# Kernel tuning notes

Measured on AMD Instinct MI355X. Metric: run time of the kernel, lower is better.

The kernel has to match this reference:

```python
import jax, jax.numpy as jnp
import numpy as np

# ---- static config (mirrors HashEncoderHyFluid.__init__) ----
MIN_RES = np.array([16, 16, 16, 16], dtype=np.float64)
MAX_RES = np.array([256, 256, 256, 128], dtype=np.float64)
NUM_SCALES = 16
MAX_PARAMS = 2 ** 19
F = 2  # features_per_level
N_QUERIES = 1_000_000
PRIMES = np.array([1, 2654435761, 805459861, 3674653429], dtype=np.uint32)
# 16 corner offsets of the 4D hypercube, bit d of idx selects low/high along dim d
BITS = np.array([[(i >> d) & 1 for d in range(4)] for i in range(16)], dtype=np.int32)  # (16,4)


def build_config():
    b = np.exp((np.log(MAX_RES) - np.log(MIN_RES)) / (NUM_SCALES - 1))
    shapes, sizes, indicators, offsets = [], [], [], []
    total = 0
    for s in range(NUM_SCALES):
        res = np.ceil(MIN_RES * np.power(b, s)).astype(np.int64)
        raw = int(res[0] + 1) * int(res[1] + 1) * int(res[2] + 1) * int(res[3] + 1)
        p = raw if raw % 8 == 0 else ((raw + 7) // 8) * 8
        p = min(MAX_PARAMS, p)
        shapes.append(res)
        sizes.append(p)
        indicators.append(1 if raw <= p else 0)
        offsets.append(total)
        total += p * F
    return shapes, sizes, indicators, offsets, total


SHAPES, SIZES, INDICATORS, OFFSETS, TOTAL_HASH_SIZE = build_config()  # total = 15205344


def setup_inputs() -> dict:
    key = jax.random.key(0)
    k1, k2 = jax.random.split(key)
    xyzt = jax.random.uniform(k1, (N_QUERIES, 4), dtype=jnp.float32)  # coords in [0,1)
    hash_table = (jax.random.uniform(k2, (TOTAL_HASH_SIZE,), dtype=jnp.float32) * 2.0 - 1.0) * 0.001
    return {"xyzt": xyzt, "hash_table": hash_table}


def _encode_scale(xyzt, hash_table, res, size, indicator, offset):
    # xyzt: (N,4) in [0,1]; res: np int64 (4,)
    resf = jnp.asarray(res.astype(np.float32))
    pos = xyzt * resf                      # (N,4) grid-space position
    grid = jnp.floor(pos)
    frac = pos - grid                      # (N,4)
    grid = grid.astype(jnp.int32)
    corners = grid[:, None, :] + jnp.asarray(BITS)[None, :, :]          # (N,16,4)
    hi = jnp.asarray(BITS, jnp.float32)[None, :, :]                     # (1,16,4)
    w = jnp.prod(hi * frac[:, None, :] + (1.0 - hi) * (1.0 - frac[:, None, :]), axis=-1)  # (N,16)
    cu = corners.astype(jnp.uint32)
    if indicator == 1:
        # dense linear indexing: strides = cumprod(res+1), wrapping at uint32 like taichi
        strides = np.cumprod(np.concatenate([[1], (res + 1)[:3]])).astype(np.uint32)
        idx = jnp.sum(cu * jnp.asarray(strides), axis=-1)               # (N,16) uint32, wraps
    else:
        # xor hash with large primes
        h = cu[..., 0] * jnp.uint32(PRIMES[0])
        for d in range(1, 4):
            h = h ^ (cu[..., d] * jnp.uint32(PRIMES[d]))
        idx = h
    idx = (idx % jnp.uint32(size)).astype(jnp.int32)
    base = offset + idx * F                                             # (N,16)
    feats = hash_table[base[..., None] + jnp.arange(F)]                 # (N,16,F)
    return jnp.einsum("nc,ncf->nf", w, feats)                           # (N,F)


def reference(xyzt, hash_table):
    outs = []
    for s in range(NUM_SCALES):
        outs.append(_encode_scale(xyzt, hash_table, SHAPES[s], SIZES[s], INDICATORS[s], OFFSETS[s]))
    return jnp.concatenate(outs, axis=-1)  # (N, NUM_SCALES * F)
```

## Files before the change

kernel.cpp:

```cpp
#include <hip/hip_runtime.h>
#include <cstdint>
#include <cmath>


#define NSCALES 16
#define TPB 256
#define BINS 65536

struct Cfg {
  float    res[NSCALES][4];
  uint32_t key[NSCALES][4];
  uint32_t mask[NSCALES];
  int      offset[NSCALES];
  int      dense[NSCALES];
};

typedef float v4f __attribute__((ext_vector_type(4)));
typedef float v2f __attribute__((ext_vector_type(2)));

__device__ __forceinline__ uint32_t bucket_key(float x, float y, float z, float w)
{
  uint32_t bx = (uint32_t)(x * 16.f); bx = bx > 15u ? 15u : bx;
  uint32_t by = (uint32_t)(y * 16.f); by = by > 15u ? 15u : by;
  uint32_t bz = (uint32_t)(z * 16.f); bz = bz > 15u ? 15u : bz;
  uint32_t bt = (uint32_t)(w * 16.f); bt = bt > 15u ? 15u : bt;
  uint32_t k = 0;
#pragma unroll
  for (int b = 0; b < 4; ++b) {
    k |= ((bx >> b) & 1u) << (4 * b + 0);
    k |= ((by >> b) & 1u) << (4 * b + 1);
    k |= ((bz >> b) & 1u) << (4 * b + 2);
    k |= ((bt >> b) & 1u) << (4 * b + 3);
  }
  return k;
}

__global__ __launch_bounds__(TPB) void hist_kernel(
    const float* __restrict__ xyzt, uint32_t* __restrict__ hist, int N)
{
  const int i = blockIdx.x * TPB + threadIdx.x;
  if (i >= N) return;
  const v4f c = *(reinterpret_cast<const v4f*>(xyzt) + i);
  atomicAdd(&hist[bucket_key(c.x, c.y, c.z, c.w)], 1u);
}

__global__ __launch_bounds__(256) void scan_kernel(
    const uint32_t* __restrict__ hist, uint32_t* __restrict__ boff)
{
  __shared__ uint32_t part[256];
  const int t = threadIdx.x;
  const int base = t * (BINS / 256);
  uint32_t s = 0;
  for (int j = 0; j < BINS / 256; ++j) s += hist[base + j];
  part[t] = s;
  __syncthreads();
  for (int off = 1; off < 256; off <<= 1) {
    uint32_t v = (t >= off) ? part[t - off] : 0u;
    __syncthreads();
    part[t] += v;
    __syncthreads();
  }
  uint32_t run = part[t] - s;
  for (int j = 0; j < BINS / 256; ++j) {
    boff[base + j] = run;
    run += hist[base + j];
  }
}

__global__ __launch_bounds__(TPB) void scatter_kernel(
    const float* __restrict__ xyzt,
    const uint32_t* __restrict__ boff, uint32_t* __restrict__ cur,
    uint32_t* __restrict__ perm, float* __restrict__ c_sorted, int N)
{
  const int i = blockIdx.x * TPB + threadIdx.x;
  if (i >= N) return;
  const v4f c = *(reinterpret_cast<const v4f*>(xyzt) + i);
  const uint32_t k = bucket_key(c.x, c.y, c.z, c.w);
  const uint32_t pos = boff[k] + atomicAdd(&cur[k], 1u);
  perm[pos] = (uint32_t)i;
  *(reinterpret_cast<v4f*>(c_sorted) + pos) = c;
}

__global__ __launch_bounds__(TPB) void gather_kernel(
    const float*  __restrict__ coords,
    const float*  __restrict__ table,
    float2*       __restrict__ ws,
    int N, Cfg cfg)
{
  const int s = blockIdx.y;
  const int q = blockIdx.x * TPB + threadIdx.x;
  if (q >= N) return;
  const v4f c = *(reinterpret_cast<const v4f*>(coords) + q);

  const float rx = cfg.res[s][0], ry = cfg.res[s][1];
  const float rz = cfg.res[s][2], rw = cfg.res[s][3];
  const uint32_t K0 = cfg.key[s][0], K1 = cfg.key[s][1];
  const uint32_t K2 = cfg.key[s][2], K3 = cfg.key[s][3];

  const float px = c.x * rx, py = c.y * ry, pz = c.z * rz, pw = c.w * rw;
  const float gx = floorf(px), gy = floorf(py), gz = floorf(pz), gw = floorf(pw);
  const float fx = px - gx, fy = py - gy, fz = pz - gz, fw = pw - gw;
  const uint32_t ix = (uint32_t)(int)gx, iy = (uint32_t)(int)gy;
  const uint32_t iz = (uint32_t)(int)gz, iw = (uint32_t)(int)gw;

  const uint32_t x0 = ix * K0, x1 = x0 + K0;
  const uint32_t y0 = iy * K1, y1 = y0 + K1;
  const uint32_t z0 = iz * K2, z1 = z0 + K2;
  const uint32_t u0 = iw * K3, u1 = u0 + K3;

  const float wx0 = 1.f - fx, wy0 = 1.f - fy, wz0 = 1.f - fz, ww0 = 1.f - fw;
  const float wA[4] = { wx0 * wy0, fx * wy0, wx0 * fy, fx * fy };
  const float wB[4] = { wz0 * ww0, fz * ww0, wz0 * fw, fz * fw };

  const float*  tbf = table + cfg.offset[s];
  const float2* __restrict__ tb  = reinterpret_cast<const float2*>(tbf);
  const float4* __restrict__ tb4 = reinterpret_cast<const float4*>(tbf);

  float a0 = 0.f, a1 = 0.f;
  if (cfg.dense[s]) {
    const uint32_t hA[4] = { x0 + y0, x1 + y0, x0 + y1, x1 + y1 };
    const uint32_t hB[4] = { z0 + u0, z1 + u0, z0 + u1, z1 + u1 };
#pragma unroll
    for (int i = 0; i < 16; ++i) {
      const uint32_t idx = hA[i & 3] + hB[i >> 2];
      const float2 v = tb[idx];
      const float w = wA[i & 3] * wB[i >> 2];
      a0 = fmaf(w, v.x, a0);
      a1 = fmaf(w, v.y, a1);
    }
  } else {
    const uint32_t msk = cfg.mask[s];
    if ((ix & 1u) == 0u) {
      const uint32_t yv[2] = { y0, y1 };
      const uint32_t zw[4] = { z0 ^ u0, z1 ^ u0, z0 ^ u1, z1 ^ u1 };
#pragma unroll
      for (int j = 0; j < 8; ++j) {
        const int jy = j & 1, jz = j >> 1;
        const uint32_t p  = (x0 ^ yv[jy] ^ zw[jz]) & msk;
        const uint32_t e  = p & ~1u;
        const uint32_t sel = p & 1u;
        const float4 v = tb4[e >> 1];
        const float wlo = wA[2 * jy]     * wB[jz];
        const float whi = wA[2 * jy + 1] * wB[jz];
        const float l0 = sel ? v.z : v.x, l1 = sel ? v.w : v.y;
        const float h0 = sel ? v.x : v.z, h1 = sel ? v.y : v.w;
        a0 = fmaf(wlo, l0, fmaf(whi, h0, a0));
        a1 = fmaf(wlo, l1, fmaf(whi, h1, a1));
      }
    } else {
      const uint32_t hA[4] = { x0 ^ y0, x1 ^ y0, x0 ^ y1, x1 ^ y1 };
      const uint32_t hB[4] = { z0 ^ u0, z1 ^ u0, z0 ^ u1, z1 ^ u1 };
#pragma unroll
      for (int i = 0; i < 16; ++i) {
        const uint32_t idx = (hA[i & 3] ^ hB[i >> 2]) & msk;
        const float2 v = tb[idx];
        const float w = wA[i & 3] * wB[i >> 2];
        a0 = fmaf(w, v.x, a0);
        a1 = fmaf(w, v.y, a1);
      }
    }
  }
  v2f val = { a0, a1 };
  __builtin_nontemporal_store(val, (v2f*)&ws[(size_t)s * N + q]);
}

__global__ __launch_bounds__(TPB) void transpose_direct(
    const float2*   __restrict__ ws,
    const uint32_t* __restrict__ perm,
    float*          __restrict__ out,
    int N)
{
  const int g = blockIdx.x * TPB + threadIdx.x;
  if (g >= N * 8) return;
  const int q  = g >> 3;
  const int l8 = g & 7;
  const int s0 = l8 * 2;
  const float2 a = ws[(size_t)s0 * N + q];
  const float2 b = ws[(size_t)(s0 + 1) * N + q];
  const uint32_t pq = perm[q];
  v4f val = { a.x, a.y, b.x, b.y };
  __builtin_nontemporal_store(val, (v4f*)(out + (size_t)pq * 32 + l8 * 4));
}

__global__ __launch_bounds__(TPB) void transpose_kernel(
    const float2* __restrict__ ws,
    float*        __restrict__ out,
    int N)
{
  __shared__ float2 st[NSCALES][TPB + 1];
  const int t  = threadIdx.x;
  const int q  = blockIdx.x * TPB + t;
  const int ql = q < N ? q : N - 1;
#pragma unroll
  for (int s = 0; s < NSCALES; ++s)
    st[s][t] = ws[(size_t)s * N + ql];
  __syncthreads();
  const int base = blockIdx.x * (TPB * 2 * NSCALES);
#pragma unroll
  for (int it = 0; it < 8; ++it) {
    const int G  = it * 1024 + t * 4;
    const int qi = G >> 5;
    const int s0 = (G & 31) >> 1;
    if (blockIdx.x * TPB + qi < N) {
      const float2 a = st[s0][qi];
      const float2 b = st[s0 + 1][qi];
      v4f val = { a.x, a.y, b.x, b.y };
      __builtin_nontemporal_store(val, (v4f*)(out + base + G));
    }
  }
}

__global__ __launch_bounds__(TPB) void hashenc_fused(
    const float4* __restrict__ xyzt,
    const float*  __restrict__ table,
    float*        __restrict__ out,
    int N, Cfg cfg)
{
  __shared__ float2 st[NSCALES][TPB + 1];
  const int t  = threadIdx.x;
  const int q  = blockIdx.x * TPB + t;
  const int ql = q < N ? q : N - 1;
  const float4 c = xyzt[ql];
#pragma unroll 1
  for (int s = 0; s < NSCALES; ++s) {
    const float rx = cfg.res[s][0], ry = cfg.res[s][1];
    const float rz = cfg.res[s][2], rw = cfg.res[s][3];
    const uint32_t K0 = cfg.key[s][0], K1 = cfg.key[s][1];
    const uint32_t K2 = cfg.key[s][2], K3 = cfg.key[s][3];
    const float px = c.x * rx, py = c.y * ry, pz = c.z * rz, pw = c.w * rw;
    const float gx = floorf(px), gy = floorf(py), gz = floorf(pz), gw = floorf(pw);
    const float fx = px - gx, fy = py - gy, fz = pz - gz, fw = pw - gw;
    const uint32_t ix = (uint32_t)(int)gx, iy = (uint32_t)(int)gy;
    const uint32_t iz = (uint32_t)(int)gz, iw = (uint32_t)(int)gw;
    const uint32_t x0 = ix * K0, x1 = x0 + K0;
    const uint32_t y0 = iy * K1, y1 = y0 + K1;
    const uint32_t z0 = iz * K2, z1 = z0 + K2;
    const uint32_t u0 = iw * K3, u1 = u0 + K3;
    const float wx0 = 1.f - fx, wy0 = 1.f - fy, wz0 = 1.f - fz, ww0 = 1.f - fw;
    const float wA[4] = { wx0 * wy0, fx * wy0, wx0 * fy, fx * fy };
    const float wB[4] = { wz0 * ww0, fz * ww0, wz0 * fw, fz * fw };
    const float2* __restrict__ tb =
        reinterpret_cast<const float2*>(table + cfg.offset[s]);
    float a0 = 0.f, a1 = 0.f;
    if (cfg.dense[s]) {
      const uint32_t hA[4] = { x0 + y0, x1 + y0, x0 + y1, x1 + y1 };
      const uint32_t hB[4] = { z0 + u0, z1 + u0, z0 + u1, z1 + u1 };
#pragma unroll
      for (int i = 0; i < 16; ++i) {
        const uint32_t idx = hA[i & 3] + hB[i >> 2];
        const float2 v = tb[idx];
        const float w = wA[i & 3] * wB[i >> 2];
        a0 = fmaf(w, v.x, a0); a1 = fmaf(w, v.y, a1);
      }
    } else {
      const uint32_t msk = cfg.mask[s];
      const uint32_t hA[4] = { x0 ^ y0, x1 ^ y0, x0 ^ y1, x1 ^ y1 };
      const uint32_t hB[4] = { z0 ^ u0, z1 ^ u0, z0 ^ u1, z1 ^ u1 };
#pragma unroll
      for (int i = 0; i < 16; ++i) {
        const uint32_t idx = (hA[i & 3] ^ hB[i >> 2]) & msk;
        const float2 v = tb[idx];
        const float w = wA[i & 3] * wB[i >> 2];
        a0 = fmaf(w, v.x, a0); a1 = fmaf(w, v.y, a1);
      }
    }
    st[s][t] = make_float2(a0, a1);
  }
  __syncthreads();
  const int base = blockIdx.x * (TPB * 2 * NSCALES);
#pragma unroll
  for (int it = 0; it < 8; ++it) {
    const int G  = it * 1024 + t * 4;
    const int qi = G >> 5;
    const int s0 = (G & 31) >> 1;
    if (blockIdx.x * TPB + qi < N) {
      const float2 a = st[s0][qi];
      const float2 b = st[s0 + 1][qi];
      v4f val = { a.x, a.y, b.x, b.y };
      __builtin_nontemporal_store(val, (v4f*)(out + base + G));
    }
  }
}

static void build_cfg(Cfg& cfg)
{
  const double minr[4] = { 16.0, 16.0, 16.0, 16.0 };
  const double maxr[4] = { 256.0, 256.0, 256.0, 128.0 };
  const uint32_t primes[4] = { 1u, 2654435761u, 805459861u, 3674653429u };

  double b[4];
  for (int d = 0; d < 4; ++d)
    b[d] = ::exp((::log(maxr[d]) - ::log(minr[d])) / (double)(NSCALES - 1));

  long long total = 0;
  for (int s = 0; s < NSCALES; ++s) {
    long long res[4];
    for (int d = 0; d < 4; ++d)
      res[d] = (long long)::ceil(minr[d] * ::pow(b[d], (double)s));

    const long long raw =
        (res[0] + 1) * (res[1] + 1) * (res[2] + 1) * (res[3] + 1);
    long long p = (raw % 8 == 0) ? raw : ((raw + 7) / 8) * 8;
    if (p > 524288) p = 524288;
    const int ind = (raw <= p) ? 1 : 0;

    for (int d = 0; d < 4; ++d) cfg.res[s][d] = (float)res[d];
    if (ind) {
      cfg.key[s][0] = 1u;
      cfg.key[s][1] = (uint32_t)(res[0] + 1);
      cfg.key[s][2] = (uint32_t)((res[0] + 1) * (res[1] + 1));
      cfg.key[s][3] = (uint32_t)((res[0] + 1) * (res[1] + 1) * (res[2] + 1));
    } else {
      for (int d = 0; d < 4; ++d) cfg.key[s][d] = primes[d];
    }
    cfg.mask[s]   = (uint32_t)(p - 1);
    cfg.offset[s] = (int)total;
    cfg.dense[s]  = ind;
    total += p * 2;
  }
}

static inline size_t align_up(size_t v, size_t a) { return (v + a - 1) & ~(a - 1); }

extern "C" void kernel_launch(void* const* d_in, const int* in_sizes, int n_in,
                              void* d_out, int out_size, void* d_ws, size_t ws_size,
                              hipStream_t stream)
{
  const float* xyzt  = (const float*)d_in[0];
  const float* table = (const float*)d_in[1];
  float*       out   = (float*)d_out;
  const int N = in_sizes[0] / 4;

  Cfg cfg;
  build_cfg(cfg);

  const int qblocks = (N + TPB - 1) / TPB;

  size_t off = 0;
  const size_t perm_off = off;             off = align_up(off + (size_t)N * 4, 256);
  const size_t hist_off = off;             off = align_up(off + (size_t)BINS * 4, 256);
  const size_t cur_off  = off;             off = align_up(off + (size_t)BINS * 4, 256);
  const size_t boff_off = off;             off = align_up(off + (size_t)BINS * 4, 256);
  const size_t cs_off   = align_up(off, 16);  off = cs_off + (size_t)N * 16;
  const size_t ws_off   = align_up(off, 16);
  const size_t need_sorted = ws_off + (size_t)N * NSCALES * sizeof(float2);
  const size_t need_plain  = (size_t)N * NSCALES * sizeof(float2);

  char* wsb = (char*)d_ws;

  if (ws_size >= need_sorted) {
    uint32_t* perm = (uint32_t*)(wsb + perm_off);
    uint32_t* hist = (uint32_t*)(wsb + hist_off);
    uint32_t* cur  = (uint32_t*)(wsb + cur_off);
    uint32_t* boff = (uint32_t*)(wsb + boff_off);
    float*    csrt = (float*)(wsb + cs_off);
    float2*   ws   = (float2*)(wsb + ws_off);

    hipMemsetAsync(hist, 0, (size_t)BINS * 4, stream);
    hipMemsetAsync(cur,  0, (size_t)BINS * 4, stream);
    hipLaunchKernelGGL(hist_kernel, dim3(qblocks), dim3(TPB), 0, stream,
                       xyzt, hist, N);
    hipLaunchKernelGGL(scan_kernel, dim3(1), dim3(256), 0, stream, hist, boff);
    hipLaunchKernelGGL(scatter_kernel, dim3(qblocks), dim3(TPB), 0, stream,
                       xyzt, boff, cur, perm, csrt, N);
    hipLaunchKernelGGL(gather_kernel, dim3(qblocks, NSCALES), dim3(TPB), 0,
                       stream, csrt, table, ws, N, cfg);
    const int tblocks = (N * 8 + TPB - 1) / TPB;
    hipLaunchKernelGGL(transpose_direct, dim3(tblocks), dim3(TPB), 0, stream,
                       ws, perm, out, N);
  } else if (ws_size >= need_plain) {
    float2* ws = (float2*)d_ws;
    hipLaunchKernelGGL(gather_kernel, dim3(qblocks, NSCALES), dim3(TPB), 0,
                       stream, xyzt, table, ws, N, cfg);
    hipLaunchKernelGGL(transpose_kernel, dim3(qblocks), dim3(TPB), 0,
                       stream, ws, out, N);
  } else {
    hipLaunchKernelGGL(hashenc_fused, dim3(qblocks), dim3(TPB), 0,
                       stream, (const float4*)xyzt, table, out, N, cfg);
  }
}
```

Measured before the change: 841.0 us.

## Stage per-bucket hash-table neighborhoods in LDS for the coarse scales

Adds a bucket_kernel in which one wave handles one spatial bucket of sorted queries. For the first six coarse scales it loads that bucket's grid-cell neighbourhood of table entries into shared memory once, then interpolates every query in the bucket from LDS, falling back to global gathers when a query lies outside the staged region. The remaining scales still use the original gather kernel, now launched with a scale base offset. The scan kernel is also widened to 1024 threads. The aim is to stop repeated global-memory gathers at coarse levels, where many queries share corners, at the cost of wave-level load imbalance (bucket counts vary) and an extra kernel launch.

```diff
diff --git a/kernel.cpp b/kernel.cpp
--- a/kernel.cpp
+++ b/kernel.cpp
@@ -6,6 +6,9 @@
 #define NSCALES 16
 #define TPB 256
 #define BINS 65536
+#define WPB 4
+#define SCAP 512
+#define NSB 6
 
 struct Cfg {
   float    res[NSCALES][4];
@@ -44,24 +47,24 @@
   atomicAdd(&hist[bucket_key(c.x, c.y, c.z, c.w)], 1u);
 }
 
-__global__ __launch_bounds__(256) void scan_kernel(
+__global__ __launch_bounds__(1024) void scan_kernel(
     const uint32_t* __restrict__ hist, uint32_t* __restrict__ boff)
 {
-  __shared__ uint32_t part[256];
+  __shared__ uint32_t part[1024];
   const int t = threadIdx.x;
-  const int base = t * (BINS / 256);
+  const int base = t * (BINS / 1024);
   uint32_t s = 0;
-  for (int j = 0; j < BINS / 256; ++j) s += hist[base + j];
+  for (int j = 0; j < BINS / 1024; ++j) s += hist[base + j];
   part[t] = s;
   __syncthreads();
-  for (int off = 1; off < 256; off <<= 1) {
+  for (int off = 1; off < 1024; off <<= 1) {
     uint32_t v = (t >= off) ? part[t - off] : 0u;
     __syncthreads();
     part[t] += v;
     __syncthreads();
   }
   uint32_t run = part[t] - s;
-  for (int j = 0; j < BINS / 256; ++j) {
+  for (int j = 0; j < BINS / 1024; ++j) {
     boff[base + j] = run;
     run += hist[base + j];
   }
@@ -81,13 +84,157 @@
   *(reinterpret_cast<v4f*>(c_sorted) + pos) = c;
 }
 
+__global__ __launch_bounds__(TPB) void bucket_kernel(
+    const float*    __restrict__ coords,
+    const float*    __restrict__ table,
+    const uint32_t* __restrict__ hist,
+    const uint32_t* __restrict__ boff,
+    float2*         __restrict__ ws,
+    int N, Cfg cfg)
+{
+  __shared__ float2 S[WPB][SCAP];
+  const int wave = threadIdx.x >> 6;
+  const int lane = threadIdx.x & 63;
+  const uint32_t k = (uint32_t)blockIdx.x * WPB + (uint32_t)wave;
+
+  int bc[4];
+#pragma unroll
+  for (int d = 0; d < 4; ++d) {
+    uint32_t v = 0;
+#pragma unroll
+    for (int b = 0; b < 4; ++b) v |= ((k >> (4 * b + d)) & 1u) << b;
+    bc[d] = (int)v;
+  }
+  const uint32_t cnt   = hist[k];
+  const uint32_t start = boff[k];
+
+#pragma unroll 1
+  for (int s = 0; s < NSB; ++s) {
+    const float rx = cfg.res[s][0], ry = cfg.res[s][1];
+    const float rz = cfg.res[s][2], rw = cfg.res[s][3];
+    const uint32_t K0 = cfg.key[s][0], K1 = cfg.key[s][1];
+    const uint32_t K2 = cfg.key[s][2], K3 = cfg.key[s][3];
+    const uint32_t msk = cfg.mask[s];
+    const int dense = cfg.dense[s];
+    const float2* __restrict__ tb =
+        reinterpret_cast<const float2*>(table + cfg.offset[s]);
+
+    int plo[4], pc[4];
+#pragma unroll
+    for (int d = 0; d < 4; ++d) {
+      const int R  = (int)cfg.res[s][d];
+      const int lo = (bc[d] * R) >> 4;
+      const int hi = ((bc[d] + 1) * R - 1) >> 4;
+      plo[d] = lo;
+      pc[d]  = hi - lo + 2;
+    }
+    const int pcx = pc[0], pcy = pc[1], pcz = pc[2];
+    const int tot = pcx * pcy * pcz * pc[3];
+    const bool staged = (tot <= SCAP);
+
+    if (staged) {
+      for (int e = lane; e < tot; e += 64) {
+        int t = e;
+        const int ex = t % pcx; t /= pcx;
+        const int ey = t % pcy; t /= pcy;
+        const int ez = t % pcz; t /= pcz;
+        const int ew = t;
+        const uint32_t X = (uint32_t)(plo[0] + ex) * K0;
+        const uint32_t Y = (uint32_t)(plo[1] + ey) * K1;
+        const uint32_t Z = (uint32_t)(plo[2] + ez) * K2;
+        const uint32_t W = (uint32_t)(plo[3] + ew) * K3;
+        const uint32_t idx = dense ? (X + Y + Z + W)
+                                   : ((X ^ Y ^ Z ^ W) & msk);
+        S[wave][e] = tb[idx];
+      }
+    }
+    __syncthreads();
+
+    for (uint32_t base = 0; base < cnt; base += 64u) {
+      const uint32_t qi = base + (uint32_t)lane;
+      if (qi < cnt) {
+        const int q = (int)(start + qi);
+        const v4f c = *(reinterpret_cast<const v4f*>(coords) + q);
+        const float px = c.x * rx, py = c.y * ry, pz = c.z * rz, pw = c.w * rw;
+        const float gx = floorf(px), gy = floorf(py);
+        const float gz = floorf(pz), gw = floorf(pw);
+        const float fx = px - gx, fy = py - gy, fz = pz - gz, fw = pw - gw;
+        const int ix = (int)gx, iy = (int)gy, iz = (int)gz, iw = (int)gw;
+        const float wx0 = 1.f - fx, wy0 = 1.f - fy;
+        const float wz0 = 1.f - fz, ww0 = 1.f - fw;
+
+        const int lx = ix - plo[0], ly = iy - plo[1];
+        const int lz = iz - plo[2], lw = iw - plo[3];
+        const bool ok = staged &&
+            (unsigned)lx <= (unsigned)(pcx - 2) &&
+            (unsigned)ly <= (unsigned)(pcy - 2) &&
+            (unsigned)lz <= (unsigned)(pcz - 2) &&
+            (unsigned)lw <= (unsigned)(pc[3] - 2);
+
+        float a0 = 0.f, a1 = 0.f;
+        if (ok) {
+          const float wyv[2] = { wy0, fy };
+          const float wzv[2] = { wz0, fz };
+          const float wwv[2] = { ww0, fw };
+          const int b0 = lx + pcx * (ly + pcy * (lz + pcz * lw));
+#pragma unroll
+          for (int jw = 0; jw < 2; ++jw)
+#pragma unroll
+            for (int jz = 0; jz < 2; ++jz)
+#pragma unroll
+              for (int jy = 0; jy < 2; ++jy) {
+                const int o = b0 + pcx * (jy + pcy * (jz + pcz * jw));
+                const float2 v0 = S[wave][o];
+                const float2 v1 = S[wave][o + 1];
+                const float wv = wyv[jy] * wzv[jz] * wwv[jw];
+                a0 = fmaf(wv, fmaf(wx0, v0.x, fx * v1.x), a0);
+                a1 = fmaf(wv, fmaf(wx0, v0.y, fx * v1.y), a1);
+              }
+        } else {
+          const uint32_t X0 = (uint32_t)ix * K0, X1 = X0 + K0;
+          const uint32_t Y0 = (uint32_t)iy * K1, Y1 = Y0 + K1;
+          const uint32_t Z0 = (uint32_t)iz * K2, Z1 = Z0 + K2;
+          const uint32_t U0 = (uint32_t)iw * K3, U1 = U0 + K3;
+          const float wAv[4] = { wx0 * wy0, fx * wy0, wx0 * fy, fx * fy };
+          const float wBv[4] = { wz0 * ww0, fz * ww0, wz0 * fw, fz * fw };
+          uint32_t hA[4], hB[4];
+          if (dense) {
+            hA[0] = X0 + Y0; hA[1] = X1 + Y0; hA[2] = X0 + Y1; hA[3] = X1 + Y1;
+            hB[0] = Z0 + U0; hB[1] = Z1 + U0; hB[2] = Z0 + U1; hB[3] = Z1 + U1;
+#pragma unroll
+            for (int i = 0; i < 16; ++i) {
+              const uint32_t idx = hA[i & 3] + hB[i >> 2];
+              const float2 v = tb[idx];
+              const float w = wAv[i & 3] * wBv[i >> 2];
+              a0 = fmaf(w, v.x, a0); a1 = fmaf(w, v.y, a1);
+            }
+          } else {
+            hA[0] = X0 ^ Y0; hA[1] = X1 ^ Y0; hA[2] = X0 ^ Y1; hA[3] = X1 ^ Y1;
+            hB[0] = Z0 ^ U0; hB[1] = Z1 ^ U0; hB[2] = Z0 ^ U1; hB[3] = Z1 ^ U1;
+#pragma unroll
+            for (int i = 0; i < 16; ++i) {
+              const uint32_t idx = (hA[i & 3] ^ hB[i >> 2]) & msk;
+              const float2 v = tb[idx];
+              const float w = wAv[i & 3] * wBv[i >> 2];
+              a0 = fmaf(w, v.x, a0); a1 = fmaf(w, v.y, a1);
+            }
+          }
+        }
+        v2f val = { a0, a1 };
+        __builtin_nontemporal_store(val, (v2f*)&ws[(size_t)s * N + q]);
+      }
+    }
+    __syncthreads();
+  }
+}
+
 __global__ __launch_bounds__(TPB) void gather_kernel(
     const float*  __restrict__ coords,
     const float*  __restrict__ table,
     float2*       __restrict__ ws,
-    int N, Cfg cfg)
-{
-  const int s = blockIdx.y;
+    int N, int s_base, Cfg cfg)
+{
+  const int s = (int)blockIdx.y + s_base;
   const int q = blockIdx.x * TPB + threadIdx.x;
   if (q >= N) return;
   const v4f c = *(reinterpret_cast<const v4f*>(coords) + q);
@@ -360,18 +507,20 @@
     hipMemsetAsync(cur,  0, (size_t)BINS * 4, stream);
     hipLaunchKernelGGL(hist_kernel, dim3(qblocks), dim3(TPB), 0, stream,
                        xyzt, hist, N);
-    hipLaunchKernelGGL(scan_kernel, dim3(1), dim3(256), 0, stream, hist, boff);
+    hipLaunchKernelGGL(scan_kernel, dim3(1), dim3(1024), 0, stream, hist, boff);
     hipLaunchKernelGGL(scatter_kernel, dim3(qblocks), dim3(TPB), 0, stream,
                        xyzt, boff, cur, perm, csrt, N);
-    hipLaunchKernelGGL(gather_kernel, dim3(qblocks, NSCALES), dim3(TPB), 0,
-                       stream, csrt, table, ws, N, cfg);
+    hipLaunchKernelGGL(bucket_kernel, dim3(BINS / WPB), dim3(TPB), 0, stream,
+                       csrt, table, hist, boff, ws, N, cfg);
+    hipLaunchKernelGGL(gather_kernel, dim3(qblocks, NSCALES - NSB), dim3(TPB),
+                       0, stream, csrt, table, ws, N, NSB, cfg);
     const int tblocks = (N * 8 + TPB - 1) / TPB;
     hipLaunchKernelGGL(transpose_direct, dim3(tblocks), dim3(TPB), 0, stream,
                        ws, perm, out, N);
   } else if (ws_size >= need_plain) {
     float2* ws = (float2*)d_ws;
     hipLaunchKernelGGL(gather_kernel, dim3(qblocks, NSCALES), dim3(TPB), 0,
-                       stream, xyzt, table, ws, N, cfg);
+                       stream, xyzt, table, ws, N, 0, cfg);
     hipLaunchKernelGGL(transpose_kernel, dim3(qblocks), dim3(TPB), 0,
                        stream, ws, out, N);
   } else {
```

Result: slower. 1.033 ms (+22.8%).
